# Optimization experiments

Measured on AMD Instinct MI355X. Metric: run time of the kernel, lower is better.

The kernel has to match this reference:

```python
import jax, jax.numpy as jnp
import numpy as np
from jax import lax

# bior3.5 decomposition low-pass filter (pywt.Wavelet('bior3.5').dec_lo)
_BIOR35_DEC_LO = [-0.013810679320049757, 0.04143203796014927, 0.052480581416189075,
                  -0.26792717880896527, -0.07181553246425873, 0.966747552403483,
                  0.966747552403483, -0.07181553246425873, -0.26792717880896527,
                  0.052480581416189075, 0.04143203796014927, -0.013810679320049757]

J = 3  # decomposition levels


def setup_inputs() -> dict:
    key = jax.random.key(0)
    x = jax.random.normal(key, (16, 64, 16384), dtype=jnp.float32)
    hac = jnp.asarray(np.array(_BIOR35_DEC_LO, dtype=np.float32))
    return {"x": x, "hac": hac}


def _afb1d(x, h0, h1):
    """Analysis filter bank: stride-2 depthwise conv over last dim.

    x: (B, C, N); h0, h1: (L,). Returns (lo, hi), each (B, C, outsize).
    Since every channel uses the same pair of filters, we fold (B, C) into
    the batch dim and run a single-input-channel, 2-output-channel conv.
    """
    B, C, N = x.shape
    L = h0.shape[0]
    outsize = (N + L - 1) // 2              # pywt 'zero' mode coeff length
    p = 2 * (outsize - 1) - N + L           # total padding needed
    if p % 2 == 1:                          # odd -> extra zero on the right
        x = jnp.pad(x, ((0, 0), (0, 0), (0, 1)))
        N += 1
        p -= 1
    half = p // 2
    xr = x.reshape(B * C, 1, N)
    k = jnp.stack([h0, h1])[:, None, :]     # (2, 1, L) -- cross-correlation, like torch
    out = lax.conv_general_dilated(xr, k, window_strides=(2,),
                                   padding=[(half, half)],
                                   dimension_numbers=('NCH', 'OIH', 'NCH'))
    lo = out[:, 0, :].reshape(B, C, outsize)
    hi = out[:, 1, :].reshape(B, C, outsize)
    return lo, hi


def reference(x, hac):
    L = hac.shape[0]
    # QMF pair: h1[i] = (-1)^(i+1) * h0[L-1-i]  (miu[::2] = -1 in torch code)
    sign = jnp.where(jnp.arange(L) % 2 == 0, -1.0, 1.0).astype(hac.dtype)
    h0 = hac
    h1 = hac[::-1] * sign
    x0 = x
    highs = []
    for _ in range(J):
        x0, x1 = _afb1d(x0, h0, h1)
        highs.append(x1)
    return (x0, *highs)
```

## Files before the change

### kernel.cpp

```cpp
#include <hip/hip_runtime.h>


#define FILT_LEN 12
#define ROWS  1024
#define N1    16384
#define O1    8197
#define O2    4104
#define O3    2057
#define NBLK  8
#define T1    1025
#define T2    513
#define T3    258
#define NTHR  256

#define XCAP    2208
#define L1CAP   1120
#define LO2_OFF 1088
#define LO2SZ   560
#define HB2_OFF 1664
#define HI3_OFF 272

constexpr int cmin(int a, int b) { return a < b ? a : b; }
constexpr int cmax(int a, int b) { return a > b ? a : b; }

__device__ __forceinline__ int sw4(int f4) { return f4 ^ ((f4 >> 3) & 7); }
__device__ __forceinline__ float4 ld4(const float* p, int f4) {
    return reinterpret_cast<const float4*>(p)[sw4(f4)];
}
__device__ __forceinline__ void st4(float* p, int f4, float4 v) {
    reinterpret_cast<float4*>(p)[sw4(f4)] = v;
}
__device__ __forceinline__ float ldss(const float* p, int j) {
    return p[(sw4(j >> 2) << 2) | (j & 3)];
}
__device__ __forceinline__ void stss(float* p, int j, float v) {
    p[(sw4(j >> 2) << 2) | (j & 3)] = v;
}

__device__ __forceinline__ void bar_lgkm() {
    asm volatile("s_waitcnt lgkmcnt(0)" ::: "memory");
    __builtin_amdgcn_s_barrier();
    asm volatile("" ::: "memory");
}

__device__ __forceinline__ void ntst(float* p, float v) {
    __builtin_nontemporal_store(v, p);
}

__device__ __forceinline__ constexpr float h0tap(int i) {
    constexpr float H[FILT_LEN] = {
        -0.013810679320049757f, 0.04143203796014927f, 0.052480581416189075f,
        -0.26792717880896527f, -0.07181553246425873f, 0.966747552403483f,
        0.966747552403483f, -0.07181553246425873f, -0.26792717880896527f,
        0.052480581416189075f, 0.04143203796014927f, -0.013810679320049757f};
    return H[i];
}
__device__ __forceinline__ constexpr float h1tap(int i) {
    return h0tap(FILT_LEN - 1 - i) * ((i & 1) ? 1.0f : -1.0f);
}

template<int B>
struct Cfg {
    static constexpr int s1 = B * T1, e1 = cmin(s1 + T1, O1);
    static constexpr int s2 = B * T2, e2 = cmin(s2 + T2, O2);
    static constexpr int s3 = B * T3, e3 = cmin(s3 + T3, O3);
    static constexpr int c2s = cmax(0, cmin(s2, 2 * s3 - 10)) & ~1;
    static constexpr int c2e = cmin(O2, cmax(e2, 2 * e3));
    static constexpr int c1s = cmax(0, cmin(s1, 2 * c2s - 10)) & ~1;
    static constexpr int c1e = cmin(O1, cmax(e1, 2 * c2e));
    static constexpr int span1 = c1e - c1s;
    static constexpr int span2 = c2e - c2s;
    static constexpr int span3 = e3 - s3;
    static constexpr int xbase = 2 * c1s - 12;
    static constexpr int D2 = 2 * c2s - 10 - c1s + 12;
    static constexpr int ab2 = D2 & ~3, p2 = D2 & 3;
    static constexpr int D3 = 2 * s3 - 10 - c2s + 12;
    static constexpr int ab3 = D3 & ~3, p3 = D3 & 3;
    static constexpr int zt1 = L1CAP - (12 + span1);
    static constexpr int zt2 = LO2SZ - (12 + span2);
    static constexpr int o1s = s1 - c1s, o1e = e1 - c1s;
    static constexpr int o2s = s2 - c2s, o2e = e2 - c2s;

    static_assert(D2 >= 0 && D3 >= 0, "pad origin");
    static_assert((D2 & 1) == 0 && (D3 & 1) == 0, "window parity (R5 bug)");
    static_assert(p2 <= 2 && p3 <= 2, "window shift fits 28-float window");
    static_assert((xbase & 3) == 0, "x staging alignment");
    static_assert(zt1 >= 0 && zt1 <= NTHR, "l1 tail zero in one pass");
    static_assert(zt2 >= 0 && zt2 <= NTHR, "lo2 tail zero in one pass");
    static_assert(span1 <= 8 * NTHR && span2 <= 8 * NTHR && span3 <= 8 * NTHR,
                  "single K=8 pass");
    static_assert(2 * (((span1 - 1) / 8) * 8) + 25 + 2 < XCAP, "L1 window read");
    static_assert(2 * (((span2 - 1) / 8) * 8) + ab2 + 25 + p2 < L1CAP, "L2 window read");
    static_assert(2 * (((span3 - 1) / 8) * 8) + ab3 + 25 + p3 < LO2SZ, "L3 window read");
    static_assert(span1 <= LO2_OFF, "hi1 stash fits");
    static_assert(HB2_OFF + span2 <= XCAP, "hi2 stash fits");
    static_assert(HI3_OFF + span3 <= L1CAP, "hi3 stash fits");
    static_assert(HI3_OFF >= span3, "lo3/hi3 disjoint");
};

template<int B>
__device__ __forceinline__ void body(
    const float* __restrict__ xrow,
    float* __restrict__ lo3r, float* __restrict__ hi1r,
    float* __restrict__ hi2r, float* __restrict__ hi3r,
    float* __restrict__ xs, float* __restrict__ l1, const int tid)
{
    using C = Cfg<B>;

    if constexpr (C::xbase >= 0 && C::xbase + XCAP <= N1) {
        st4(xs, tid,       *reinterpret_cast<const float4*>(xrow + C::xbase + 4 * tid));
        st4(xs, tid + 256, *reinterpret_cast<const float4*>(xrow + C::xbase + 1024 + 4 * tid));
        if (tid < XCAP / 4 - 512)
            st4(xs, tid + 512, *reinterpret_cast<const float4*>(xrow + C::xbase + 2048 + 4 * tid));
    } else {
        for (int i = tid; i < XCAP / 4; i += NTHR) {
            const int g0 = C::xbase + 4 * i;
            float4 v;
            if (g0 >= 0 && g0 + 4 <= N1) {
                v = *reinterpret_cast<const float4*>(xrow + g0);
            } else {
                v.x = ((unsigned)(g0 + 0) < (unsigned)N1) ? xrow[g0 + 0] : 0.f;
                v.y = ((unsigned)(g0 + 1) < (unsigned)N1) ? xrow[g0 + 1] : 0.f;
                v.z = ((unsigned)(g0 + 2) < (unsigned)N1) ? xrow[g0 + 2] : 0.f;
                v.w = ((unsigned)(g0 + 3) < (unsigned)N1) ? xrow[g0 + 3] : 0.f;
            }
            st4(xs, i, v);
        }
    }
    if (tid < 12)      stss(l1, tid, 0.f);
    if (tid < C::zt1)  stss(l1, 12 + C::span1 + tid, 0.f);
    bar_lgkm();

    float hr1[8];
    const int tt1 = tid * 8;
    if (tt1 < C::span1) {
        float w[28];
#pragma unroll
        for (int m = 0; m < 7; ++m) {
            const float4 v = ld4(xs, tid * 4 + m);
            w[4 * m + 0] = v.x; w[4 * m + 1] = v.y;
            w[4 * m + 2] = v.z; w[4 * m + 3] = v.w;
        }
        float a0[8];
#pragma unroll
        for (int k = 0; k < 8; ++k) { a0[k] = 0.f; hr1[k] = 0.f; }
#pragma unroll
        for (int l = 0; l < FILT_LEN; ++l) {
#pragma unroll
            for (int k = 0; k < 8; ++k) {
                const float v = w[2 * k + 2 + l];
                a0[k]  = fmaf(v, h0tap(l), a0[k]);
                hr1[k] = fmaf(v, h1tap(l), hr1[k]);
            }
        }
        if (tt1 + 8 <= C::span1) {
            st4(l1, 3 + 2 * tid, make_float4(a0[0], a0[1], a0[2], a0[3]));
            st4(l1, 4 + 2 * tid, make_float4(a0[4], a0[5], a0[6], a0[7]));
        } else {
#pragma unroll
            for (int k = 0; k < 8; ++k)
                if (tt1 + k < C::span1) stss(l1, 12 + tt1 + k, a0[k]);
        }
    }
    bar_lgkm();

    if (tt1 < C::span1) {
        if (tt1 + 8 <= C::span1) {
            st4(xs, 2 * tid,     make_float4(hr1[0], hr1[1], hr1[2], hr1[3]));
            st4(xs, 2 * tid + 1, make_float4(hr1[4], hr1[5], hr1[6], hr1[7]));
        } else {
#pragma unroll
            for (int k = 0; k < 8; ++k)
                if (tt1 + k < C::span1) stss(xs, tt1 + k, hr1[k]);
        }
    }
    if (tid < 12)      stss(xs, LO2_OFF + tid, 0.f);
    if (tid < C::zt2)  stss(xs, LO2_OFF + 12 + C::span2 + tid, 0.f);

    {
        const int tt2 = tid * 8;
        if (tt2 < C::span2) {
            float w[28];
#pragma unroll
            for (int m = 0; m < 7; ++m) {
                const float4 v = ld4(l1, tid * 4 + (C::ab2 >> 2) + m);
                w[4 * m + 0] = v.x; w[4 * m + 1] = v.y;
                w[4 * m + 2] = v.z; w[4 * m + 3] = v.w;
            }
            float a0[8], a1[8];
#pragma unroll
            for (int k = 0; k < 8; ++k) { a0[k] = 0.f; a1[k] = 0.f; }
#pragma unroll
            for (int l = 0; l < FILT_LEN; ++l) {
#pragma unroll
                for (int k = 0; k < 8; ++k) {
                    const float v = w[2 * k + l + C::p2];
                    a0[k] = fmaf(v, h0tap(l), a0[k]);
                    a1[k] = fmaf(v, h1tap(l), a1[k]);
                }
            }
            if (tt2 + 8 <= C::span2) {
                st4(xs, 275 + 2 * tid, make_float4(a0[0], a0[1], a0[2], a0[3]));
                st4(xs, 276 + 2 * tid, make_float4(a0[4], a0[5], a0[6], a0[7]));
                st4(xs, 416 + 2 * tid, make_float4(a1[0], a1[1], a1[2], a1[3]));
                st4(xs, 417 + 2 * tid, make_float4(a1[4], a1[5], a1[6], a1[7]));
            } else {
#pragma unroll
                for (int k = 0; k < 8; ++k) {
                    if (tt2 + k < C::span2) {
                        stss(xs, LO2_OFF + 12 + tt2 + k, a0[k]);
                        stss(xs, HB2_OFF + tt2 + k, a1[k]);
                    }
                }
            }
        }
    }
    bar_lgkm();

    for (int i = C::o1s + tid; i < C::o1e; i += NTHR)
        ntst(hi1r + C::c1s + i, ldss(xs, i));
    for (int i = C::o2s + tid; i < C::o2e; i += NTHR)
        ntst(hi2r + C::c2s + i, ldss(xs, HB2_OFF + i));

    {
        const int tt3 = tid * 8;
        if (tt3 < C::span3) {
            float w[28];
#pragma unroll
            for (int m = 0; m < 7; ++m) {
                const float4 v = ld4(xs, (LO2_OFF >> 2) + tid * 4 + (C::ab3 >> 2) + m);
                w[4 * m + 0] = v.x; w[4 * m + 1] = v.y;
                w[4 * m + 2] = v.z; w[4 * m + 3] = v.w;
            }
            float a0[8], a1[8];
#pragma unroll
            for (int k = 0; k < 8; ++k) { a0[k] = 0.f; a1[k] = 0.f; }
#pragma unroll
            for (int l = 0; l < FILT_LEN; ++l) {
#pragma unroll
                for (int k = 0; k < 8; ++k) {
                    const float v = w[2 * k + l + C::p3];
                    a0[k] = fmaf(v, h0tap(l), a0[k]);
                    a1[k] = fmaf(v, h1tap(l), a1[k]);
                }
            }
            if (tt3 + 8 <= C::span3) {
                st4(l1, 2 * tid,                     make_float4(a0[0], a0[1], a0[2], a0[3]));
                st4(l1, 2 * tid + 1,                 make_float4(a0[4], a0[5], a0[6], a0[7]));
                st4(l1, (HI3_OFF >> 2) + 2 * tid,     make_float4(a1[0], a1[1], a1[2], a1[3]));
                st4(l1, (HI3_OFF >> 2) + 2 * tid + 1, make_float4(a1[4], a1[5], a1[6], a1[7]));
            } else {
#pragma unroll
                for (int k = 0; k < 8; ++k) {
                    if (tt3 + k < C::span3) {
                        stss(l1, tt3 + k, a0[k]);
                        stss(l1, HI3_OFF + tt3 + k, a1[k]);
                    }
                }
            }
        }
    }
    bar_lgkm();

    for (int i = tid; i < C::span3; i += NTHR) {
        ntst(lo3r + C::s3 + i, ldss(l1, i));
        ntst(hi3r + C::s3 + i, ldss(l1, HI3_OFF + i));
    }
}

__global__ __launch_bounds__(NTHR, 8) void dwt_fused_kernel(
    const float* __restrict__ x,
    float* __restrict__ lo3, float* __restrict__ hi1,
    float* __restrict__ hi2, float* __restrict__ hi3)
{
    __shared__ __align__(16) float xs[XCAP];
    __shared__ __align__(16) float l1[L1CAP];

    const int tile = blockIdx.y & 7;
    const int row  = (int)blockIdx.x * 128 + ((int)blockIdx.y >> 3);
    const int tid = threadIdx.x;
    const float* xrow = x + (size_t)row * N1;
    float* lo3r = lo3 + (size_t)row * O3;
    float* hi1r = hi1 + (size_t)row * O1;
    float* hi2r = hi2 + (size_t)row * O2;
    float* hi3r = hi3 + (size_t)row * O3;

    switch (tile) {
        case 0:  body<0>(xrow, lo3r, hi1r, hi2r, hi3r, xs, l1, tid); break;
        case 1:  body<1>(xrow, lo3r, hi1r, hi2r, hi3r, xs, l1, tid); break;
        case 2:  body<2>(xrow, lo3r, hi1r, hi2r, hi3r, xs, l1, tid); break;
        case 3:  body<3>(xrow, lo3r, hi1r, hi2r, hi3r, xs, l1, tid); break;
        case 4:  body<4>(xrow, lo3r, hi1r, hi2r, hi3r, xs, l1, tid); break;
        case 5:  body<5>(xrow, lo3r, hi1r, hi2r, hi3r, xs, l1, tid); break;
        case 6:  body<6>(xrow, lo3r, hi1r, hi2r, hi3r, xs, l1, tid); break;
        default: body<7>(xrow, lo3r, hi1r, hi2r, hi3r, xs, l1, tid); break;
    }
}

extern "C" void kernel_launch(void* const* d_in, const int* in_sizes, int n_in,
                              void* d_out, int out_size, void* d_ws, size_t ws_size,
                              hipStream_t stream)
{
    const float* x = (const float*)d_in[0];
    float* out = (float*)d_out;

    float* lo3 = out;
    float* hi1 = out + (size_t)ROWS * O3;
    float* hi2 = hi1 + (size_t)ROWS * O1;
    float* hi3 = hi2 + (size_t)ROWS * O2;

    dwt_fused_kernel<<<dim3(NBLK, ROWS), dim3(NTHR), 0, stream>>>(
        x, lo3, hi1, hi2, hi3);
}
```

Measured before the change: 119.7 us.

## Store high bands directly from registers with vector nontemporal stores

High-pass outputs of all three levels, and the level-3 low band, are now written straight from registers to global memory using 16- or 8-byte nontemporal stores. Previously they were staged through LDS and copied out with scalar stores. This drops the LDS round trips, the scalar copy loops and one barrier. Tile starts are aligned to multiples of 4 so the vector stores line up, at the cost of slightly wider overlap spans. Per-thread stores now cover 8 consecutive elements, so each wavefront's global writes are strided rather than fully coalesced.

```diff
diff --git a/kernel.cpp b/kernel.cpp
--- a/kernel.cpp
+++ b/kernel.cpp
@@ -17,8 +17,9 @@
 #define L1CAP   1120
 #define LO2_OFF 1088
 #define LO2SZ   560
-#define HB2_OFF 1664
-#define HI3_OFF 272
+
+typedef float vf4 __attribute__((ext_vector_type(4)));
+typedef float vf2 __attribute__((ext_vector_type(2)));
 
 constexpr int cmin(int a, int b) { return a < b ? a : b; }
 constexpr int cmax(int a, int b) { return a > b ? a : b; }
@@ -45,6 +46,14 @@
 
 __device__ __forceinline__ void ntst(float* p, float v) {
     __builtin_nontemporal_store(v, p);
+}
+__device__ __forceinline__ void ntst2(float* p, float a, float b) {
+    vf2 v; v.x = a; v.y = b;
+    __builtin_nontemporal_store(v, reinterpret_cast<vf2*>(p));
+}
+__device__ __forceinline__ void ntst4(float* p, float a, float b, float c, float d) {
+    vf4 v; v.x = a; v.y = b; v.z = c; v.w = d;
+    __builtin_nontemporal_store(v, reinterpret_cast<vf4*>(p));
 }
 
 __device__ __forceinline__ constexpr float h0tap(int i) {
@@ -64,9 +73,9 @@
     static constexpr int s1 = B * T1, e1 = cmin(s1 + T1, O1);
     static constexpr int s2 = B * T2, e2 = cmin(s2 + T2, O2);
     static constexpr int s3 = B * T3, e3 = cmin(s3 + T3, O3);
-    static constexpr int c2s = cmax(0, cmin(s2, 2 * s3 - 10)) & ~1;
+    static constexpr int c2s = cmax(0, cmin(s2, 2 * s3 - 10)) & ~3;
     static constexpr int c2e = cmin(O2, cmax(e2, 2 * e3));
-    static constexpr int c1s = cmax(0, cmin(s1, 2 * c2s - 10)) & ~1;
+    static constexpr int c1s = cmax(0, cmin(s1, 2 * c2s - 10)) & ~3;
     static constexpr int c1e = cmin(O1, cmax(e1, 2 * c2e));
     static constexpr int span1 = c1e - c1s;
     static constexpr int span2 = c2e - c2s;
@@ -84,6 +93,7 @@
     static_assert(D2 >= 0 && D3 >= 0, "pad origin");
     static_assert((D2 & 1) == 0 && (D3 & 1) == 0, "window parity (R5 bug)");
     static_assert(p2 <= 2 && p3 <= 2, "window shift fits 28-float window");
+    static_assert((c1s & 3) == 0 && (c2s & 3) == 0, "hi-band store alignment");
     static_assert((xbase & 3) == 0, "x staging alignment");
     static_assert(zt1 >= 0 && zt1 <= NTHR, "l1 tail zero in one pass");
     static_assert(zt2 >= 0 && zt2 <= NTHR, "lo2 tail zero in one pass");
@@ -92,10 +102,7 @@
     static_assert(2 * (((span1 - 1) / 8) * 8) + 25 + 2 < XCAP, "L1 window read");
     static_assert(2 * (((span2 - 1) / 8) * 8) + ab2 + 25 + p2 < L1CAP, "L2 window read");
     static_assert(2 * (((span3 - 1) / 8) * 8) + ab3 + 25 + p3 < LO2SZ, "L3 window read");
-    static_assert(span1 <= LO2_OFF, "hi1 stash fits");
-    static_assert(HB2_OFF + span2 <= XCAP, "hi2 stash fits");
-    static_assert(HI3_OFF + span3 <= L1CAP, "hi3 stash fits");
-    static_assert(HI3_OFF >= span3, "lo3/hi3 disjoint");
+    static_assert(o1e <= span1 && o2e <= span2, "owned range inside span");
 };
 
 template<int B>
@@ -131,52 +138,51 @@
     if (tid < C::zt1)  stss(l1, 12 + C::span1 + tid, 0.f);
     bar_lgkm();
 
-    float hr1[8];
-    const int tt1 = tid * 8;
-    if (tt1 < C::span1) {
-        float w[28];
-#pragma unroll
-        for (int m = 0; m < 7; ++m) {
-            const float4 v = ld4(xs, tid * 4 + m);
-            w[4 * m + 0] = v.x; w[4 * m + 1] = v.y;
-            w[4 * m + 2] = v.z; w[4 * m + 3] = v.w;
+    {
+        const int tt1 = tid * 8;
+        if (tt1 < C::span1) {
+            float w[28];
+#pragma unroll
+            for (int m = 0; m < 7; ++m) {
+                const float4 v = ld4(xs, tid * 4 + m);
+                w[4 * m + 0] = v.x; w[4 * m + 1] = v.y;
+                w[4 * m + 2] = v.z; w[4 * m + 3] = v.w;
+            }
+            float a0[8], a1[8];
+#pragma unroll
+            for (int k = 0; k < 8; ++k) { a0[k] = 0.f; a1[k] = 0.f; }
+#pragma unroll
+            for (int l = 0; l < FILT_LEN; ++l) {
+#pragma unroll
+                for (int k = 0; k < 8; ++k) {
+                    const float v = w[2 * k + 2 + l];
+                    a0[k] = fmaf(v, h0tap(l), a0[k]);
+                    a1[k] = fmaf(v, h1tap(l), a1[k]);
+                }
+            }
+            if (tt1 + 8 <= C::span1) {
+                st4(l1, 3 + 2 * tid, make_float4(a0[0], a0[1], a0[2], a0[3]));
+                st4(l1, 4 + 2 * tid, make_float4(a0[4], a0[5], a0[6], a0[7]));
+            } else {
+#pragma unroll
+                for (int k = 0; k < 8; ++k)
+                    if (tt1 + k < C::span1) stss(l1, 12 + tt1 + k, a0[k]);
+            }
+            if (tt1 >= C::o1s && tt1 + 8 <= C::o1e) {
+                ntst4(hi1r + C::c1s + tt1,     a1[0], a1[1], a1[2], a1[3]);
+                ntst4(hi1r + C::c1s + tt1 + 4, a1[4], a1[5], a1[6], a1[7]);
+            } else {
+#pragma unroll
+                for (int k = 0; k < 8; ++k)
+                    if (tt1 + k >= C::o1s && tt1 + k < C::o1e)
+                        ntst(hi1r + C::c1s + tt1 + k, a1[k]);
+            }
         }
-        float a0[8];
-#pragma unroll
-        for (int k = 0; k < 8; ++k) { a0[k] = 0.f; hr1[k] = 0.f; }
-#pragma unroll
-        for (int l = 0; l < FILT_LEN; ++l) {
-#pragma unroll
-            for (int k = 0; k < 8; ++k) {
-                const float v = w[2 * k + 2 + l];
-                a0[k]  = fmaf(v, h0tap(l), a0[k]);
-                hr1[k] = fmaf(v, h1tap(l), hr1[k]);
-            }
-        }
-        if (tt1 + 8 <= C::span1) {
-            st4(l1, 3 + 2 * tid, make_float4(a0[0], a0[1], a0[2], a0[3]));
-            st4(l1, 4 + 2 * tid, make_float4(a0[4], a0[5], a0[6], a0[7]));
-        } else {
-#pragma unroll
-            for (int k = 0; k < 8; ++k)
-                if (tt1 + k < C::span1) stss(l1, 12 + tt1 + k, a0[k]);
-        }
     }
     bar_lgkm();
 
-    if (tt1 < C::span1) {
-        if (tt1 + 8 <= C::span1) {
-            st4(xs, 2 * tid,     make_float4(hr1[0], hr1[1], hr1[2], hr1[3]));
-            st4(xs, 2 * tid + 1, make_float4(hr1[4], hr1[5], hr1[6], hr1[7]));
-        } else {
-#pragma unroll
-            for (int k = 0; k < 8; ++k)
-                if (tt1 + k < C::span1) stss(xs, tt1 + k, hr1[k]);
-        }
-    }
     if (tid < 12)      stss(xs, LO2_OFF + tid, 0.f);
     if (tid < C::zt2)  stss(xs, LO2_OFF + 12 + C::span2 + tid, 0.f);
-
     {
         const int tt2 = tid * 8;
         if (tt2 < C::span2) {
@@ -202,25 +208,23 @@
             if (tt2 + 8 <= C::span2) {
                 st4(xs, 275 + 2 * tid, make_float4(a0[0], a0[1], a0[2], a0[3]));
                 st4(xs, 276 + 2 * tid, make_float4(a0[4], a0[5], a0[6], a0[7]));
-                st4(xs, 416 + 2 * tid, make_float4(a1[0], a1[1], a1[2], a1[3]));
-                st4(xs, 417 + 2 * tid, make_float4(a1[4], a1[5], a1[6], a1[7]));
-            } else {
-#pragma unroll
-                for (int k = 0; k < 8; ++k) {
-                    if (tt2 + k < C::span2) {
-                        stss(xs, LO2_OFF + 12 + tt2 + k, a0[k]);
-                        stss(xs, HB2_OFF + tt2 + k, a1[k]);
-                    }
-                }
+            } else {
+#pragma unroll
+                for (int k = 0; k < 8; ++k)
+                    if (tt2 + k < C::span2) stss(xs, LO2_OFF + 12 + tt2 + k, a0[k]);
+            }
+            if (tt2 >= C::o2s && tt2 + 8 <= C::o2e) {
+                ntst4(hi2r + C::c2s + tt2,     a1[0], a1[1], a1[2], a1[3]);
+                ntst4(hi2r + C::c2s + tt2 + 4, a1[4], a1[5], a1[6], a1[7]);
+            } else {
+#pragma unroll
+                for (int k = 0; k < 8; ++k)
+                    if (tt2 + k >= C::o2s && tt2 + k < C::o2e)
+                        ntst(hi2r + C::c2s + tt2 + k, a1[k]);
             }
         }
     }
     bar_lgkm();
-
-    for (int i = C::o1s + tid; i < C::o1e; i += NTHR)
-        ntst(hi1r + C::c1s + i, ldss(xs, i));
-    for (int i = C::o2s + tid; i < C::o2e; i += NTHR)
-        ntst(hi2r + C::c2s + i, ldss(xs, HB2_OFF + i));
 
     {
         const int tt3 = tid * 8;
@@ -245,26 +249,28 @@
                 }
             }
             if (tt3 + 8 <= C::span3) {
-                st4(l1, 2 * tid,                     make_float4(a0[0], a0[1], a0[2], a0[3]));
-                st4(l1, 2 * tid + 1,                 make_float4(a0[4], a0[5], a0[6], a0[7]));
-                st4(l1, (HI3_OFF >> 2) + 2 * tid,     make_float4(a1[0], a1[1], a1[2], a1[3]));
-                st4(l1, (HI3_OFF >> 2) + 2 * tid + 1, make_float4(a1[4], a1[5], a1[6], a1[7]));
+                if constexpr ((C::s3 & 3) == 0) {
+                    ntst4(lo3r + C::s3 + tt3,     a0[0], a0[1], a0[2], a0[3]);
+                    ntst4(lo3r + C::s3 + tt3 + 4, a0[4], a0[5], a0[6], a0[7]);
+                    ntst4(hi3r + C::s3 + tt3,     a1[0], a1[1], a1[2], a1[3]);
+                    ntst4(hi3r + C::s3 + tt3 + 4, a1[4], a1[5], a1[6], a1[7]);
+                } else {
+#pragma unroll
+                    for (int q = 0; q < 4; ++q) {
+                        ntst2(lo3r + C::s3 + tt3 + 2 * q, a0[2 * q], a0[2 * q + 1]);
+                        ntst2(hi3r + C::s3 + tt3 + 2 * q, a1[2 * q], a1[2 * q + 1]);
+                    }
+                }
             } else {
 #pragma unroll
                 for (int k = 0; k < 8; ++k) {
                     if (tt3 + k < C::span3) {
-                        stss(l1, tt3 + k, a0[k]);
-                        stss(l1, HI3_OFF + tt3 + k, a1[k]);
+                        ntst(lo3r + C::s3 + tt3 + k, a0[k]);
+                        ntst(hi3r + C::s3 + tt3 + k, a1[k]);
                     }
                 }
             }
         }
-    }
-    bar_lgkm();
-
-    for (int i = tid; i < C::span3; i += NTHR) {
-        ntst(lo3r + C::s3 + i, ldss(l1, i));
-        ntst(hi3r + C::s3 + i, ldss(l1, HI3_OFF + i));
     }
 }
 
```

Result: slower. 126.2 us (+5.5%).
